# Performance work log

Measured on AMD Instinct MI355X. Metric: run time of the kernel, lower is better.

Reference implementation:

```python
import jax, jax.numpy as jnp
import numpy as np

HEADS = 16
NEG_INF = -1e30


def rel_shift(t):
    # t: [b, h, i, j] with i == j; Transformer-XL style relative shift
    b, h, i, j = t.shape
    t = jnp.pad(t, ((0, 0), (0, 0), (0, 0), (1, 0)))  # zero pad on last dim front
    t = t.reshape(b, h, j + 1, i)[:, :, 1:]
    return t.reshape(b, h, i, j)


def setup_inputs() -> dict:
    key = jax.random.key(0)
    ks = jax.random.split(key, 8)
    b, n, dim = 2, 2048, 1024
    d_head = dim // HEADS
    w = 0.02
    return {
        "x": jax.random.normal(ks[0], (b, n, dim), dtype=jnp.float32),
        "pos_emb": jax.random.normal(ks[1], (n, dim), dtype=jnp.float32),
        "Wq": jax.random.normal(ks[2], (dim, dim), dtype=jnp.float32) * w,
        "bq": jnp.zeros((dim,), dtype=jnp.float32),
        "Wkv": jax.random.normal(ks[3], (dim, 2 * dim), dtype=jnp.float32) * w,
        "bkv": jnp.zeros((2 * dim,), dtype=jnp.float32),
        "Wp": jax.random.normal(ks[4], (dim, d_head), dtype=jnp.float32) * w,
        "bp": jnp.zeros((d_head,), dtype=jnp.float32),
        "Wo": jax.random.normal(ks[5], (dim, dim), dtype=jnp.float32) * w,
        "bo": jnp.zeros((dim,), dtype=jnp.float32),
    }


def reference(x, pos_emb, Wq, bq, Wkv, bkv, Wp, bp, Wo, bo):
    b, n, dim = x.shape
    h = HEADS
    d = dim // h
    scale = d ** -0.5

    q = (x @ Wq + bq).reshape(b, n, h, d).transpose(0, 2, 1, 3)  # b h n d
    kv = x @ Wkv + bkv
    k, v = jnp.split(kv, 2, axis=-1)
    k = k.reshape(b, n, h, d).transpose(0, 2, 1, 3)
    v = v.reshape(b, n, h, d).transpose(0, 2, 1, 3)

    dots = jnp.einsum('bhid,bhjd->bhij', q, k) * scale

    # relative position bias
    p = pos_emb @ Wp + bp  # [n, d]
    pos_attn = jnp.einsum('bhid,jd->bhij', q, p) * scale
    dots = dots + rel_shift(pos_attn)

    # causal mask
    causal = jnp.triu(jnp.ones((n, n), dtype=bool), 1)
    dots = jnp.where(causal[None, None], NEG_INF, dots)

    attn = jax.nn.softmax(dots, axis=-1)
    out = jnp.einsum('bhij,bhjd->bhid', attn, v)
    out = out.transpose(0, 2, 1, 3).reshape(b, n, dim)
    return out @ Wo + bo
```

## Files before the change

kernel.cpp:

```cpp
#include <hip/hip_runtime.h>
#include <hip/hip_bf16.h>
#include <cstdint>
#include <cstddef>

#define SEQ_N 2048
#define DIM   1024
#define NHEAD 16
#define DH    64

typedef __bf16 bf16;
typedef __attribute__((ext_vector_type(8))) __bf16 bf16x8;
typedef __attribute__((ext_vector_type(4))) __bf16 bf16x4;
typedef __attribute__((ext_vector_type(4))) float f32x4;

__device__ __forceinline__ void gl_lds16(const bf16* g, bf16* l) {
    __builtin_amdgcn_global_load_lds(
        (const __attribute__((address_space(1))) unsigned int*)g,
        (__attribute__((address_space(3))) unsigned int*)l, 16, 0, 0);
}

__global__ __launch_bounds__(256) void prep_kernel(
    const float* __restrict__ x, const float* __restrict__ pos,
    const float* __restrict__ Wq, const float* __restrict__ Wkv,
    const float* __restrict__ Wo, const float* __restrict__ Wp,
    bf16* __restrict__ xb, bf16* __restrict__ posb,
    bf16* __restrict__ WqkvT, bf16* __restrict__ WoT, bf16* __restrict__ WpT)
{
    int bid = blockIdx.x;
    if (bid < 6144) {
        const int NX = 4096 * 1024;
        int i = (bid * 256 + threadIdx.x) * 4;
        if (i < NX) {
            float4 v = *(const float4*)&x[i];
            bf16x4 o;
            o[0] = (bf16)v.x; o[1] = (bf16)v.y; o[2] = (bf16)v.z; o[3] = (bf16)v.w;
            *(bf16x4*)&xb[i] = o;
        } else {
            int j = i - NX;
            float4 v = *(const float4*)&pos[j];
            bf16x4 o;
            o[0] = (bf16)v.x; o[1] = (bf16)v.y; o[2] = (bf16)v.z; o[3] = (bf16)v.w;
            *(bf16x4*)&posb[j] = o;
        }
        return;
    }
    __shared__ float t[32][33];
    bid -= 6144;
    const float* src; bf16* dst; int tidx, nx, N;
    if (bid < 1024)      { src = Wq;  dst = WqkvT;                       tidx = bid;        nx = 32; N = 1024; }
    else if (bid < 3072) { src = Wkv; dst = WqkvT + (size_t)1024 * 1024; tidx = bid - 1024; nx = 64; N = 2048; }
    else if (bid < 4096) { src = Wo;  dst = WoT;                         tidx = bid - 3072; nx = 32; N = 1024; }
    else                 { src = Wp;  dst = WpT;                         tidx = bid - 4096; nx = 2;  N = 64;   }
    int n0 = (tidx % nx) * 32, k0 = (tidx / nx) * 32;
    int tx = threadIdx.x & 31, ty = threadIdx.x >> 5;
    #pragma unroll
    for (int r = ty; r < 32; r += 8)
        t[r][tx] = src[(size_t)(k0 + r) * N + n0 + tx];
    __syncthreads();
    #pragma unroll
    for (int r = ty; r < 32; r += 8)
        dst[(size_t)(n0 + r) * 1024 + k0 + tx] = (bf16)t[tx][r];
}

__global__ __launch_bounds__(256) void qkvp_kernel(
    const bf16* __restrict__ xb, const bf16* __restrict__ WqkvT,
    const bf16* __restrict__ posb, const bf16* __restrict__ WpT,
    const float* __restrict__ bq, const float* __restrict__ bkv,
    const float* __restrict__ bp,
    bf16* __restrict__ qbuf, bf16* __restrict__ kbuf,
    bf16* __restrict__ vtbuf, bf16* __restrict__ pfrag)
{
    __shared__ __align__(16) bf16 sm[128 * 132];
    bf16* At = sm;
    bf16* Bt = sm + 128 * 64;
    const int tid = threadIdx.x, w = tid >> 6, lane = tid & 63;
    const int q = lane >> 4, ln15 = lane & 15;
    const int lr = lane >> 3, c_log = (lane & 7) ^ lr;
    const int f  = (int)blockIdx.x + 25 * (int)blockIdx.y;
    const int jx = f >> 3;
    const int bx = jx % 25;
    const int by = ((f & 7) << 2) + jx / 25;
    const int m0 = by * 128;

    if (bx == 24) {
        if (by >= 16) return;
        f32x4 acc[2][4] = {};
        for (int k0 = 0; k0 < 1024; k0 += 64) {
            __syncthreads();
            #pragma unroll
            for (int t = 0; t < 4; ++t)
                gl_lds16(&posb[(size_t)(m0 + 32 * w + 8 * t + lr) * 1024 + k0 + c_log * 8],
                         &At[(32 * w + 8 * t) * 64]);
            #pragma unroll
            for (int t = 0; t < 2; ++t)
                gl_lds16(&WpT[(size_t)(16 * w + 8 * t + lr) * 1024 + k0 + c_log * 8],
                         &Bt[(16 * w + 8 * t) * 64]);
            __syncthreads();
            bf16x8 bfr[2][4];
            #pragma unroll
            for (int ks = 0; ks < 2; ++ks)
                #pragma unroll
                for (int sn = 0; sn < 4; ++sn) {
                    int rb = 16 * sn + ln15;
                    bfr[ks][sn] = *(const bf16x8*)&Bt[(rb * 8 + ((4 * ks + q) ^ (rb & 7))) * 8];
                }
            #pragma unroll
            for (int sm2 = 0; sm2 < 2; ++sm2) {
                int ra = 32 * w + 16 * sm2 + ln15;
                #pragma unroll
                for (int ks = 0; ks < 2; ++ks) {
                    bf16x8 af = *(const bf16x8*)&At[(ra * 8 + ((4 * ks + q) ^ (ra & 7))) * 8];
                    #pragma unroll
                    for (int sn = 0; sn < 4; ++sn)
                        acc[sm2][sn] = __builtin_amdgcn_mfma_f32_16x16x32_bf16(
                            af, bfr[ks][sn], acc[sm2][sn], 0, 0, 0);
                }
            }
        }
        #pragma unroll
        for (int sm2 = 0; sm2 < 2; ++sm2)
            #pragma unroll
            for (int sn = 0; sn < 4; ++sn)
                #pragma unroll
                for (int r = 0; r < 4; ++r) {
                    int row = m0 + 32 * w + 16 * sm2 + 4 * q + r;
                    int d = 16 * sn + ln15;
                    int sb = row >> 4, lnp = row & 15;
                    int ks2 = d >> 5, qd = (d >> 3) & 3, e = d & 7;
                    pfrag[(((size_t)sb * 2 + ks2) * 64 + qd * 16 + lnp) * 8 + e] =
                        (bf16)(acc[sm2][sn][r] + bp[d]);
                }
        return;
    }

    const int n0 = bx * 128;
    const int wm = w >> 1, wn = w & 1;
    f32x4 acc[4][4] = {};

    for (int k0 = 0; k0 < 1024; k0 += 64) {
        __syncthreads();
        #pragma unroll
        for (int t = 0; t < 4; ++t) {
            int r = 32 * w + 8 * t + lr;
            gl_lds16(&xb[(size_t)(m0 + r) * 1024 + k0 + c_log * 8],
                     &At[(32 * w + 8 * t) * 64]);
            gl_lds16(&WqkvT[(size_t)(n0 + r) * 1024 + k0 + c_log * 8],
                     &Bt[(32 * w + 8 * t) * 64]);
        }
        __syncthreads();

        bf16x8 af[2][4], bfr[2][4];
        #pragma unroll
        for (int ks = 0; ks < 2; ++ks)
            #pragma unroll
            for (int s = 0; s < 4; ++s) {
                int ra = 64 * wm + 16 * s + ln15;
                af[ks][s]  = *(const bf16x8*)&At[(ra * 8 + ((4 * ks + q) ^ (ra & 7))) * 8];
                int rb = 64 * wn + 16 * s + ln15;
                bfr[ks][s] = *(const bf16x8*)&Bt[(rb * 8 + ((4 * ks + q) ^ (rb & 7))) * 8];
            }
        #pragma unroll
        for (int ks = 0; ks < 2; ++ks)
            #pragma unroll
            for (int si = 0; si < 4; ++si)
                #pragma unroll
                for (int sj = 0; sj < 4; ++sj)
                    acc[si][sj] = __builtin_amdgcn_mfma_f32_16x16x32_bf16(
                        af[ks][si], bfr[ks][sj], acc[si][sj], 0, 0, 0);
    }

    if (bx < 16) {
        const float QSCL = 0.125f * 1.44269504088896341f;
        #pragma unroll
        for (int si = 0; si < 4; ++si)
            #pragma unroll
            for (int sj = 0; sj < 4; ++sj)
                #pragma unroll
                for (int r = 0; r < 4; ++r) {
                    int row = m0 + 64 * wm + 16 * si + 4 * q + r;
                    int col = n0 + 64 * wn + 16 * sj + ln15;
                    float v = acc[si][sj][r] + (col < 1024 ? bq[col] : bkv[col - 1024]);
                    if (col < 1024) qbuf[(size_t)row * 1024 + col] = (bf16)(v * QSCL);
                    else            kbuf[(size_t)row * 1024 + (col - 1024)] = (bf16)v;
                }
    } else {
        __syncthreads();
        #pragma unroll
        for (int si = 0; si < 4; ++si)
            #pragma unroll
            for (int sj = 0; sj < 4; ++sj) {
                int dL = 64 * wn + 16 * sj + ln15;
                int tL = 64 * wm + 16 * si + 4 * q;
                float bias = bkv[1024 + (bx - 16) * 128 + dL];
                bf16x4 o4;
                #pragma unroll
                for (int r = 0; r < 4; ++r)
                    o4[r] = (bf16)(acc[si][sj][r] + bias);
                *(bf16x4*)&sm[dL * 132 + tL] = o4;
            }
        __syncthreads();
        const int b = m0 >> 11;
        const int t0 = m0 & 2047;
        const int h0 = (bx - 16) * 2;
        #pragma unroll
        for (int p = 0; p < 16; ++p) {
            int d = (tid >> 5) + 8 * p;
            int t = (tid & 31) * 4;
            bf16x4 v4 = *(const bf16x4*)&sm[d * 132 + t];
            int rowv = (b * NHEAD + h0 + (d >> 6)) * DH + (d & 63);
            *(bf16x4*)&vtbuf[(size_t)rowv * SEQ_N + t0 + t] = v4;
        }
    }
}

__global__ __launch_bounds__(256, 4) void attn_mfma_kernel(
    const bf16* __restrict__ qb,
    const bf16* __restrict__ kb,
    const bf16* __restrict__ vt,
    const bf16* __restrict__ pfrag,
    bf16* __restrict__ ob,
    float* __restrict__ Opart,
    float2* __restrict__ MLpart)
{
    const int f   = (int)blockIdx.x;
    const int xcd = f & 7;
    const int jj  = f >> 3;
    const int s   = jj >> 2;
    const int bh  = xcd * 4 + (jj & 3);
    int qblk, lo, hi, part;
    if (s < 16) { qblk = 16 + s; lo = 0; hi = 16; part = 0; }
    else {
        int k = (s - 16) >> 1;
        if (((s - 16) & 1) == 0) { qblk = 31 - k; lo = 16; hi = qblk + 1; part = 1; }
        else                     { qblk = 15 - k; lo = 0;  hi = qblk + 1; part = -1; }
    }
    const int bi = bh >> 4, hh = bh & 15;
    const int i0 = qblk << 6;
    const int tid = threadIdx.x, w = tid >> 6, lane = tid & 63;
    const int q = lane >> 4, ln15 = lane & 15;
    const int lr = lane >> 3, c_log = (lane & 7) ^ lr;

    __shared__ __align__(16) bf16 smem[17664];
    bf16* S2L = smem + w * 1344;
    bf16* Ks  = smem + 5376;
    bf16* Vs  = smem + 9472;
    bf16* Pw  = smem + 13568 + w * 1024;

    const bf16* qbase = qb + ((size_t)(bi * SEQ_N + i0)) * DIM + hh * DH;
    const bf16* kbase = kb + ((size_t)bi * SEQ_N) * DIM + hh * DH;
    const bf16* vbase = vt + ((size_t)(bi * NHEAD + hh) * DH) * SEQ_N;

    bf16x8 qf0 = *(const bf16x8*)&qbase[(size_t)(16 * w + ln15) * DIM + q * 8];
    bf16x8 qf1 = *(const bf16x8*)&qbase[(size_t)(16 * w + ln15) * DIM + 32 + q * 8];

    const int A0 = 127 - 4 * qblk - w;
    f32x4 s2r4;
    {
        int sb0 = A0 + 4 * lo;
        bf16x8 f0 = *(const bf16x8*)&pfrag[(((size_t)sb0 * 2 + 0) * 64 + lane) * 8];
        bf16x8 f1 = *(const bf16x8*)&pfrag[(((size_t)sb0 * 2 + 1) * 64 + lane) * 8];
        f32x4 a = {0.f, 0.f, 0.f, 0.f};
        a = __builtin_amdgcn_mfma_f32_16x16x32_bf16(f0, qf0, a, 0, 0, 0);
        a = __builtin_amdgcn_mfma_f32_16x16x32_bf16(f1, qf1, a, 0, 0, 0);
        s2r4 = a;
    }

    float m_run = -1e30f, l_run = 0.f;
    f32x4 O_T[4] = {};

    for (int jt = lo; jt < hi; ++jt) {
        const int j0 = jt << 6;

        bf16x8 pfA[4][2];
        #pragma unroll
        for (int ss = 1; ss <= 4; ++ss) {
            int sb = A0 + 4 * jt + ss;
            if (sb > 127) sb = 127;
            pfA[ss-1][0] = *(const bf16x8*)&pfrag[(((size_t)sb * 2 + 0) * 64 + lane) * 8];
            pfA[ss-1][1] = *(const bf16x8*)&pfrag[(((size_t)sb * 2 + 1) * 64 + lane) * 8];
        }
        #pragma unroll
        for (int t = 0; t < 2; ++t) {
            int r = 16 * w + 8 * t + lr;
            gl_lds16(kbase + (size_t)(j0 + r) * DIM + c_log * 8,
                     &Ks[(16 * w + 8 * t) * 64]);
            gl_lds16(vbase + (size_t)r * SEQ_N + j0 + c_log * 8,
                     &Vs[(16 * w + 8 * t) * 64]);
        }

        {
            f32x4 s2r[5];
            s2r[0] = s2r4;
            #pragma unroll
            for (int ss = 1; ss <= 4; ++ss) {
                f32x4 a = {0.f, 0.f, 0.f, 0.f};
                a = __builtin_amdgcn_mfma_f32_16x16x32_bf16(pfA[ss-1][0], qf0, a, 0, 0, 0);
                a = __builtin_amdgcn_mfma_f32_16x16x32_bf16(pfA[ss-1][1], qf1, a, 0, 0, 0);
                s2r[ss] = a;
            }
            s2r4 = s2r[4];
            #pragma unroll
            for (int ss = 0; ss < 5; ++ss)
                #pragma unroll
                for (int r = 0; r < 4; ++r)
                    S2L[ln15 * 84 + 16 * ss + 4 * q + r] = (bf16)s2r[ss][r];
        }

        __syncthreads();

        float sv[4][4];
        __builtin_amdgcn_s_setprio(1);
        #pragma unroll
        for (int sn = 0; sn < 4; ++sn) {
            int rk = 16 * sn + ln15;
            bf16x8 k0f = *(const bf16x8*)&Ks[(rk * 8 + ((q    ) ^ (rk & 7))) * 8];
            bf16x8 k1f = *(const bf16x8*)&Ks[(rk * 8 + ((4 + q) ^ (rk & 7))) * 8];
            f32x4 a;
            #pragma unroll
            for (int r = 0; r < 4; ++r)
                a[r] = (float)S2L[ln15 * 84 + 15 - ln15 + 16 * sn + 4 * q + r];
            a = __builtin_amdgcn_mfma_f32_16x16x32_bf16(k0f, qf0, a, 0, 0, 0);
            a = __builtin_amdgcn_mfma_f32_16x16x32_bf16(k1f, qf1, a, 0, 0, 0);
            #pragma unroll
            for (int r = 0; r < 4; ++r)
                sv[sn][r] = a[r];
        }
        __builtin_amdgcn_s_setprio(0);
        if (jt == qblk) {
            #pragma unroll
            for (int sn = 0; sn < 4; ++sn)
                #pragma unroll
                for (int r = 0; r < 4; ++r)
                    if (16 * sn + 4 * q + r > 16 * w + ln15)
                        sv[sn][r] = -1e30f;
        }

        float mx = sv[0][0];
        #pragma unroll
        for (int sn = 0; sn < 4; ++sn)
            #pragma unroll
            for (int r = 0; r < 4; ++r)
                mx = fmaxf(mx, sv[sn][r]);
        mx = fmaxf(mx, __shfl_xor(mx, 16));
        mx = fmaxf(mx, __shfl_xor(mx, 32));
        const float mn = fmaxf(m_run, mx);
        float sum = 0.f;
        #pragma unroll
        for (int sn = 0; sn < 4; ++sn)
            #pragma unroll
            for (int r = 0; r < 4; ++r) {
                float e = exp2f(sv[sn][r] - mn);
                sv[sn][r] = e;
                sum += e;
            }
        sum += __shfl_xor(sum, 16);
        sum += __shfl_xor(sum, 32);
        if (__all(mx <= m_run)) {
            l_run += sum;
        } else {
            const float alpha = exp2f(m_run - mn);
            l_run = l_run * alpha + sum;
            #pragma unroll
            for (int sd = 0; sd < 4; ++sd)
                #pragma unroll
                for (int r = 0; r < 4; ++r)
                    O_T[sd][r] *= alpha;
        }
        m_run = mn;

        #pragma unroll
        for (int sn = 0; sn < 4; ++sn)
            #pragma unroll
            for (int r = 0; r < 4; ++r) {
                int chunk = (2 * sn + (q >> 1)) ^ (ln15 & 7);
                Pw[ln15 * 64 + chunk * 8 + 4 * (q & 1) + r] = (bf16)sv[sn][r];
            }

        __builtin_amdgcn_s_waitcnt(0);

        __builtin_amdgcn_s_setprio(1);
        #pragma unroll
        for (int ks = 0; ks < 2; ++ks) {
            bf16x8 pT = *(const bf16x8*)&Pw[ln15 * 64 + (((4 * ks + q) ^ (ln15 & 7))) * 8];
            #pragma unroll
            for (int sd = 0; sd < 4; ++sd) {
                int rv = 16 * sd + ln15;
                bf16x8 vf = *(const bf16x8*)&Vs[(rv * 8 + ((4 * ks + q) ^ (rv & 7))) * 8];
                O_T[sd] = __builtin_amdgcn_mfma_f32_16x16x32_bf16(vf, pT, O_T[sd], 0, 0, 0);
            }
        }
        __builtin_amdgcn_s_setprio(0);
        __syncthreads();
    }

    const int row = 16 * w + ln15;
    if (part < 0) {
        const float inv = 1.0f / l_run;
        const size_t grow = (size_t)bi * SEQ_N + i0 + row;
        #pragma unroll
        for (int sd = 0; sd < 4; ++sd) {
            bf16x4 o4;
            #pragma unroll
            for (int r = 0; r < 4; ++r)
                o4[r] = (bf16)(O_T[sd][r] * inv);
            *(bf16x4*)&ob[grow * DIM + hh * DH + 16 * sd + 4 * q] = o4;
        }
    } else {
        const int slot = (bh * 16 + (qblk - 16)) * 2 + part;
        float* op = Opart + (size_t)slot * 4096 + row * 64;
        #pragma unroll
        for (int sd = 0; sd < 4; ++sd)
            *(f32x4*)&op[16 * sd + 4 * q] = O_T[sd];
        if (lane < 16)
            MLpart[slot * 64 + row] = make_float2(m_run, l_run);
    }
}

__global__ __launch_bounds__(256) void merge_kernel(
    const float* __restrict__ Opart, const float2* __restrict__ MLpart,
    bf16* __restrict__ ob)
{
    const int pb = blockIdx.x;
    const int bh = pb >> 4, qblk = 16 + (pb & 15);
    const int bi = bh >> 4, hh = bh & 15;
    const int row = threadIdx.x >> 2;
    const int d0 = (threadIdx.x & 3) * 16;

    float2 ml0 = MLpart[(pb * 2 + 0) * 64 + row];
    float2 ml1 = MLpart[(pb * 2 + 1) * 64 + row];
    float m = fmaxf(ml0.x, ml1.x);
    float a0 = exp2f(ml0.x - m), a1 = exp2f(ml1.x - m);
    float inv = 1.0f / (ml0.y * a0 + ml1.y * a1);

    const float* o0 = Opart + ((size_t)(pb * 2 + 0)) * 4096 + row * 64 + d0;
    const float* o1 = Opart + ((size_t)(pb * 2 + 1)) * 4096 + row * 64 + d0;
    bf16* dst = ob + ((size_t)(bi * SEQ_N + qblk * 64 + row)) * DIM + hh * DH + d0;
    #pragma unroll
    for (int k = 0; k < 4; ++k) {
        float4 v0 = *(const float4*)&o0[4 * k];
        float4 v1 = *(const float4*)&o1[4 * k];
        bf16x4 o4;
        o4[0] = (bf16)((v0.x * a0 + v1.x * a1) * inv);
        o4[1] = (bf16)((v0.y * a0 + v1.y * a1) * inv);
        o4[2] = (bf16)((v0.z * a0 + v1.z * a1) * inv);
        o4[3] = (bf16)((v0.w * a0 + v1.w * a1) * inv);
        *(bf16x4*)&dst[4 * k] = o4;
    }
}

__global__ __launch_bounds__(256) void outproj_kernel(
    const bf16* __restrict__ ab, const bf16* __restrict__ WoT,
    const float* __restrict__ bo, float* __restrict__ out)
{
    __shared__ __align__(16) bf16 At[128 * 64];
    __shared__ __align__(16) bf16 Bt[64 * 64];
    const int tid = threadIdx.x, w = tid >> 6, lane = tid & 63;
    const int q = lane >> 4, ln15 = lane & 15;
    const int lr = lane >> 3, c_log = (lane & 7) ^ lr;
    const int m0 = blockIdx.y * 128, n0 = blockIdx.x * 64;

    f32x4 acc[2][4] = {};
    for (int k0 = 0; k0 < 1024; k0 += 64) {
        __syncthreads();
        #pragma unroll
        for (int t = 0; t < 4; ++t)
            gl_lds16(&ab[(size_t)(m0 + 32 * w + 8 * t + lr) * 1024 + k0 + c_log * 8],
                     &At[(32 * w + 8 * t) * 64]);
        #pragma unroll
        for (int t = 0; t < 2; ++t)
            gl_lds16(&WoT[(size_t)(n0 + 16 * w + 8 * t + lr) * 1024 + k0 + c_log * 8],
                     &Bt[(16 * w + 8 * t) * 64]);
        __syncthreads();

        bf16x8 bfr[2][4];
        #pragma unroll
        for (int ks = 0; ks < 2; ++ks)
            #pragma unroll
            for (int sn = 0; sn < 4; ++sn) {
                int rb = 16 * sn + ln15;
                bfr[ks][sn] = *(const bf16x8*)&Bt[(rb * 8 + ((4 * ks + q) ^ (rb & 7))) * 8];
            }
        #pragma unroll
        for (int sm2 = 0; sm2 < 2; ++sm2) {
            int ra = 32 * w + 16 * sm2 + ln15;
            #pragma unroll
            for (int ks = 0; ks < 2; ++ks) {
                bf16x8 af = *(const bf16x8*)&At[(ra * 8 + ((4 * ks + q) ^ (ra & 7))) * 8];
                #pragma unroll
                for (int sn = 0; sn < 4; ++sn)
                    acc[sm2][sn] = __builtin_amdgcn_mfma_f32_16x16x32_bf16(
                        af, bfr[ks][sn], acc[sm2][sn], 0, 0, 0);
            }
        }
    }
    #pragma unroll
    for (int sm2 = 0; sm2 < 2; ++sm2)
        #pragma unroll
        for (int sn = 0; sn < 4; ++sn) {
            int col = n0 + 16 * sn + ln15;
            float bias = bo[col];
            #pragma unroll
            for (int r = 0; r < 4; ++r) {
                int row = m0 + 32 * w + 16 * sm2 + 4 * q + r;
                out[(size_t)row * 1024 + col] = acc[sm2][sn][r] + bias;
            }
        }
}

extern "C" void kernel_launch(void* const* d_in, const int* in_sizes, int n_in,
                              void* d_out, int out_size, void* d_ws, size_t ws_size,
                              hipStream_t stream)
{
    const float* x    = (const float*)d_in[0];
    const float* pos  = (const float*)d_in[1];
    const float* Wq   = (const float*)d_in[2];
    const float* bq   = (const float*)d_in[3];
    const float* Wkv  = (const float*)d_in[4];
    const float* bkv  = (const float*)d_in[5];
    const float* Wp   = (const float*)d_in[6];
    const float* bp   = (const float*)d_in[7];
    const float* Wo   = (const float*)d_in[8];
    const float* bo   = (const float*)d_in[9];
    float* out = (float*)d_out;

    const int M = 2 * SEQ_N;
    char* ws = (char*)d_ws;
    bf16* xb     = (bf16*)ws;  ws += (size_t)M * DIM * 2;
    bf16* posb   = (bf16*)ws;  ws += (size_t)SEQ_N * DIM * 2;
    bf16* WqkvT  = (bf16*)ws;  ws += (size_t)3072 * 1024 * 2;
    bf16* WoT    = (bf16*)ws;  ws += (size_t)DIM * DIM * 2;
    bf16* WpT    = (bf16*)ws;  ws += (size_t)DH * DIM * 2;
    bf16* qbuf   = (bf16*)ws;  ws += (size_t)M * DIM * 2;
    bf16* kbuf   = (bf16*)ws;  ws += (size_t)M * DIM * 2;
    bf16* vtbuf  = (bf16*)ws;  ws += (size_t)M * DIM * 2;
    bf16* pfrag  = (bf16*)ws;  ws += (size_t)512 * 1024;
    bf16* abuf   = (bf16*)ws;

    float*  Opart  = (float*)d_ws;
    float2* MLpart = (float2*)((char*)d_ws + (size_t)1024 * 4096 * 4);

    dim3 blk(256);
    prep_kernel<<<dim3(10304), blk, 0, stream>>>(
        x, pos, Wq, Wkv, Wo, Wp, xb, posb, WqkvT, WoT, WpT);

    qkvp_kernel<<<dim3(25, 32), blk, 0, stream>>>(
        xb, WqkvT, posb, WpT, bq, bkv, bp, qbuf, kbuf, vtbuf, pfrag);

    attn_mfma_kernel<<<dim3(1536), blk, 0, stream>>>(
        qbuf, kbuf, vtbuf, pfrag, abuf, Opart, MLpart);

    merge_kernel<<<dim3(512), blk, 0, stream>>>(Opart, MLpart, abuf);

    outproj_kernel<<<dim3(16, 32), blk, 0, stream>>>(
        abuf, WoT, bo, out);
}
```

Measured before the change: 243.3 us.

## Double-buffer LDS tiles in projection GEMMs and vectorize weight-transpose stores

The QKV/pos projection and output projection GEMM loops now use two LDS buffers. The next k-tile's global-to-LDS loads are issued before computing on the current tile, with one barrier per iteration instead of two. This aims to hide global load latency behind MFMA work. In exchange, LDS per block roughly doubles (64 KB in qkvp), which can lower occupancy. Separately, the weight-transpose prep writes four bf16 values per thread as one vector store instead of scalar stores.

```diff
diff --git a/kernel.cpp b/kernel.cpp
--- a/kernel.cpp
+++ b/kernel.cpp
@@ -57,9 +57,12 @@
     for (int r = ty; r < 32; r += 8)
         t[r][tx] = src[(size_t)(k0 + r) * N + n0 + tx];
     __syncthreads();
+    int rowi = threadIdx.x >> 3, colg = threadIdx.x & 7;
+    bf16x4 o;
     #pragma unroll
-    for (int r = ty; r < 32; r += 8)
-        dst[(size_t)(n0 + r) * 1024 + k0 + tx] = (bf16)t[tx][r];
+    for (int e = 0; e < 4; ++e)
+        o[e] = (bf16)t[colg * 4 + e][rowi];
+    *(bf16x4*)&dst[(size_t)(n0 + rowi) * 1024 + k0 + colg * 4] = o;
 }
 
 __global__ __launch_bounds__(256) void qkvp_kernel(
@@ -70,9 +73,7 @@
     bf16* __restrict__ qbuf, bf16* __restrict__ kbuf,
     bf16* __restrict__ vtbuf, bf16* __restrict__ pfrag)
 {
-    __shared__ __align__(16) bf16 sm[128 * 132];
-    bf16* At = sm;
-    bf16* Bt = sm + 128 * 64;
+    __shared__ __align__(16) bf16 sm[32768];
     const int tid = threadIdx.x, w = tid >> 6, lane = tid & 63;
     const int q = lane >> 4, ln15 = lane & 15;
     const int lr = lane >> 3, c_log = (lane & 7) ^ lr;
@@ -85,17 +86,32 @@
     if (bx == 24) {
         if (by >= 16) return;
         f32x4 acc[2][4] = {};
-        for (int k0 = 0; k0 < 1024; k0 += 64) {
-            __syncthreads();
-            #pragma unroll
-            for (int t = 0; t < 4; ++t)
-                gl_lds16(&posb[(size_t)(m0 + 32 * w + 8 * t + lr) * 1024 + k0 + c_log * 8],
-                         &At[(32 * w + 8 * t) * 64]);
-            #pragma unroll
-            for (int t = 0; t < 2; ++t)
-                gl_lds16(&WpT[(size_t)(16 * w + 8 * t + lr) * 1024 + k0 + c_log * 8],
-                         &Bt[(16 * w + 8 * t) * 64]);
-            __syncthreads();
+        #pragma unroll
+        for (int t = 0; t < 4; ++t)
+            gl_lds16(&posb[(size_t)(m0 + 32 * w + 8 * t + lr) * 1024 + c_log * 8],
+                     &sm[(32 * w + 8 * t) * 64]);
+        #pragma unroll
+        for (int t = 0; t < 2; ++t)
+            gl_lds16(&WpT[(size_t)(16 * w + 8 * t + lr) * 1024 + c_log * 8],
+                     &sm[8192 + (16 * w + 8 * t) * 64]);
+        __syncthreads();
+        int cur = 0;
+        for (int kt = 0; kt < 16; ++kt) {
+            bf16* At = sm + cur * 16384;
+            bf16* Bt = At + 8192;
+            if (kt + 1 < 16) {
+                bf16* Atn = sm + (cur ^ 1) * 16384;
+                bf16* Btn = Atn + 8192;
+                int k0 = (kt + 1) * 64;
+                #pragma unroll
+                for (int t = 0; t < 4; ++t)
+                    gl_lds16(&posb[(size_t)(m0 + 32 * w + 8 * t + lr) * 1024 + k0 + c_log * 8],
+                             &Atn[(32 * w + 8 * t) * 64]);
+                #pragma unroll
+                for (int t = 0; t < 2; ++t)
+                    gl_lds16(&WpT[(size_t)(16 * w + 8 * t + lr) * 1024 + k0 + c_log * 8],
+                             &Btn[(16 * w + 8 * t) * 64]);
+            }
             bf16x8 bfr[2][4];
             #pragma unroll
             for (int ks = 0; ks < 2; ++ks)
@@ -116,6 +132,8 @@
                             af, bfr[ks][sn], acc[sm2][sn], 0, 0, 0);
                 }
             }
+            __syncthreads();
+            cur ^= 1;
         }
         #pragma unroll
         for (int sm2 = 0; sm2 < 2; ++sm2)
@@ -137,18 +155,32 @@
     const int wm = w >> 1, wn = w & 1;
     f32x4 acc[4][4] = {};
 
-    for (int k0 = 0; k0 < 1024; k0 += 64) {
-        __syncthreads();
-        #pragma unroll
-        for (int t = 0; t < 4; ++t) {
-            int r = 32 * w + 8 * t + lr;
-            gl_lds16(&xb[(size_t)(m0 + r) * 1024 + k0 + c_log * 8],
-                     &At[(32 * w + 8 * t) * 64]);
-            gl_lds16(&WqkvT[(size_t)(n0 + r) * 1024 + k0 + c_log * 8],
-                     &Bt[(32 * w + 8 * t) * 64]);
-        }
-        __syncthreads();
-
+    #pragma unroll
+    for (int t = 0; t < 4; ++t) {
+        int r = 32 * w + 8 * t + lr;
+        gl_lds16(&xb[(size_t)(m0 + r) * 1024 + c_log * 8],
+                 &sm[(32 * w + 8 * t) * 64]);
+        gl_lds16(&WqkvT[(size_t)(n0 + r) * 1024 + c_log * 8],
+                 &sm[8192 + (32 * w + 8 * t) * 64]);
+    }
+    __syncthreads();
+    int cur = 0;
+    for (int kt = 0; kt < 16; ++kt) {
+        bf16* At = sm + cur * 16384;
+        bf16* Bt = At + 8192;
+        if (kt + 1 < 16) {
+            bf16* Atn = sm + (cur ^ 1) * 16384;
+            bf16* Btn = Atn + 8192;
+            int k0 = (kt + 1) * 64;
+            #pragma unroll
+            for (int t = 0; t < 4; ++t) {
+                int r = 32 * w + 8 * t + lr;
+                gl_lds16(&xb[(size_t)(m0 + r) * 1024 + k0 + c_log * 8],
+                         &Atn[(32 * w + 8 * t) * 64]);
+                gl_lds16(&WqkvT[(size_t)(n0 + r) * 1024 + k0 + c_log * 8],
+                         &Btn[(32 * w + 8 * t) * 64]);
+            }
+        }
         bf16x8 af[2][4], bfr[2][4];
         #pragma unroll
         for (int ks = 0; ks < 2; ++ks)
@@ -167,6 +199,8 @@
                 for (int sj = 0; sj < 4; ++sj)
                     acc[si][sj] = __builtin_amdgcn_mfma_f32_16x16x32_bf16(
                         af[ks][si], bfr[ks][sj], acc[si][sj], 0, 0, 0);
+        __syncthreads();
+        cur ^= 1;
     }
 
     if (bx < 16) {
@@ -184,7 +218,6 @@
                     else            kbuf[(size_t)row * 1024 + (col - 1024)] = (bf16)v;
                 }
     } else {
-        __syncthreads();
         #pragma unroll
         for (int si = 0; si < 4; ++si)
             #pragma unroll
@@ -452,26 +485,39 @@
     const bf16* __restrict__ ab, const bf16* __restrict__ WoT,
     const float* __restrict__ bo, float* __restrict__ out)
 {
-    __shared__ __align__(16) bf16 At[128 * 64];
-    __shared__ __align__(16) bf16 Bt[64 * 64];
+    __shared__ __align__(16) bf16 sm[24576];
     const int tid = threadIdx.x, w = tid >> 6, lane = tid & 63;
     const int q = lane >> 4, ln15 = lane & 15;
     const int lr = lane >> 3, c_log = (lane & 7) ^ lr;
     const int m0 = blockIdx.y * 128, n0 = blockIdx.x * 64;
 
     f32x4 acc[2][4] = {};
-    for (int k0 = 0; k0 < 1024; k0 += 64) {
-        __syncthreads();
-        #pragma unroll
-        for (int t = 0; t < 4; ++t)
-            gl_lds16(&ab[(size_t)(m0 + 32 * w + 8 * t + lr) * 1024 + k0 + c_log * 8],
-                     &At[(32 * w + 8 * t) * 64]);
-        #pragma unroll
-        for (int t = 0; t < 2; ++t)
-            gl_lds16(&WoT[(size_t)(n0 + 16 * w + 8 * t + lr) * 1024 + k0 + c_log * 8],
-                     &Bt[(16 * w + 8 * t) * 64]);
-        __syncthreads();
-
+    #pragma unroll
+    for (int t = 0; t < 4; ++t)
+        gl_lds16(&ab[(size_t)(m0 + 32 * w + 8 * t + lr) * 1024 + c_log * 8],
+                 &sm[(32 * w + 8 * t) * 64]);
+    #pragma unroll
+    for (int t = 0; t < 2; ++t)
+        gl_lds16(&WoT[(size_t)(n0 + 16 * w + 8 * t + lr) * 1024 + c_log * 8],
+                 &sm[8192 + (16 * w + 8 * t) * 64]);
+    __syncthreads();
+    int cur = 0;
+    for (int kt = 0; kt < 16; ++kt) {
+        bf16* At = sm + cur * 12288;
+        bf16* Bt = At + 8192;
+        if (kt + 1 < 16) {
+            bf16* Atn = sm + (cur ^ 1) * 12288;
+            bf16* Btn = Atn + 8192;
+            int k0 = (kt + 1) * 64;
+            #pragma unroll
+            for (int t = 0; t < 4; ++t)
+                gl_lds16(&ab[(size_t)(m0 + 32 * w + 8 * t + lr) * 1024 + k0 + c_log * 8],
+                         &Atn[(32 * w + 8 * t) * 64]);
+            #pragma unroll
+            for (int t = 0; t < 2; ++t)
+                gl_lds16(&WoT[(size_t)(n0 + 16 * w + 8 * t + lr) * 1024 + k0 + c_log * 8],
+                         &Btn[(16 * w + 8 * t) * 64]);
+        }
         bf16x8 bfr[2][4];
         #pragma unroll
         for (int ks = 0; ks < 2; ++ks)
@@ -492,6 +538,8 @@
                         af, bfr[ks][sn], acc[sm2][sn], 0, 0, 0);
             }
         }
+        __syncthreads();
+        cur ^= 1;
     }
     #pragma unroll
     for (int sm2 = 0; sm2 < 2; ++sm2)
```

New measurement: 232.8 us, median of 2. -4.3%, faster.
